# Optimization experiments

Measured on AMD Instinct MI355X. Metric: run time of the kernel, lower is better.

The kernel has to match this reference:

```python
import jax, jax.numpy as jnp
import numpy as np

B, L = 2, 2048          # batch, seq len (self-attention: M == L)
H, D, NB = 8, 16, 8     # n_heads, clifford_dim, n_blades (2^3 for sig_g=[1,1,1])
DM = H * D * NB         # d_model = 1024

# reverse() signs per blade for a 3D algebra, blade grades [0,1,1,1,2,2,2,3]:
# (-1)^{k(k-1)/2}; Euclidean metric signs from get_blade_signs are all +1,
# so the combined twist q_w = reverse(q) * signs is just these per-blade signs.
REV_SIGNS = jnp.array([1., 1., 1., 1., -1., -1., -1., -1.], dtype=jnp.float32)


def setup_inputs() -> dict:
    key = jax.random.key(0)
    ks = jax.random.split(key, 7)
    s = 1.0 / np.sqrt(DM)
    return {
        "query": jax.random.normal(ks[0], (B, L, DM), dtype=jnp.float32),
        "Wq": jax.random.normal(ks[1], (DM, DM), dtype=jnp.float32) * s,
        "bq": jax.random.normal(ks[2], (DM,), dtype=jnp.float32) * s,
        "Wk": jax.random.normal(ks[3], (DM, DM), dtype=jnp.float32) * s,
        "bk": jax.random.normal(ks[4], (DM,), dtype=jnp.float32) * s,
        "Wv": jax.random.normal(ks[5], (DM, DM), dtype=jnp.float32) * s,
        "bv": jax.random.normal(ks[6], (DM,), dtype=jnp.float32) * s,
    }


def reference(query, Wq, bq, Wk, bk, Wv, bv):
    b, l, _ = query.shape
    # projections (torch Linear: x @ W^T + b), reshape to (B,H,L,D,NB)
    def proj(x, W, bias):
        y = x @ W.T + bias
        return y.reshape(b, l, H, D, NB).transpose(0, 2, 1, 3, 4)

    q = proj(query, Wq, bq)
    k = proj(query, Wk, bk)   # self-attention: key = value = query
    v = proj(query, Wv, bv)

    q_w = q * REV_SIGNS  # reverse + blade-sign twist (elementwise over blade axis)
    scale = 1.0 / np.sqrt(D * NB)
    logits = jnp.einsum('bhldi,bhmdi->bhlm', q_w, k) * scale
    attn = jax.nn.softmax(logits, axis=-1)
    out = jnp.einsum('bhlm,bhmdi->bhldi', attn, v)
    out = out.transpose(0, 2, 1, 3, 4).reshape(b, l, -1)
    return out, attn.mean(axis=1)  # need_weights=True path
```

## Files before the change

kernel.cpp:

```cpp
#include <hip/hip_runtime.h>

typedef __attribute__((ext_vector_type(8))) __bf16 bf16x8;
typedef __attribute__((ext_vector_type(4))) __bf16 bf16x4;
typedef __attribute__((ext_vector_type(4))) float f32x4;
typedef __attribute__((ext_vector_type(16))) float f32x16;
typedef __attribute__((ext_vector_type(8))) unsigned short us8;
typedef __attribute__((ext_vector_type(4))) unsigned int u32x4;

constexpr float SCALE_L2E = 0.08838834764831845f * 1.4426950408889634f;

__device__ __forceinline__ unsigned short f2bf(float f) {
  unsigned int u = __float_as_uint(f);
  u = (u + 0x7FFFu + ((u >> 16) & 1u)) >> 16;
  return (unsigned short)u;
}

__device__ __forceinline__ void gl_lds16(const void* g, void* l) {
  __builtin_amdgcn_global_load_lds(
      (__attribute__((address_space(1))) void*)const_cast<void*>(g),
      (__attribute__((address_space(3))) void*)l, 16, 0, 0);
}

__global__ __launch_bounds__(256) void k_convert(
    const float* __restrict__ q, const float* __restrict__ wq,
    const float* __restrict__ wk, const float* __restrict__ wv,
    unsigned short* __restrict__ xb, unsigned short* __restrict__ wb) {
  long i = ((long)blockIdx.x * 256 + threadIdx.x) * 8;
  const float* s; unsigned short* d;
  if (i < 4194304)      { s = q  + i;             d = xb + i; }
  else if (i < 5242880) { s = wq + (i - 4194304); d = wb + (i - 4194304); }
  else if (i < 6291456) { s = wk + (i - 5242880); d = wb + 1048576 + (i - 5242880); }
  else                  { s = wv + (i - 6291456); d = wb + 2097152 + (i - 6291456); }
  float4 a = *(const float4*)s;
  float4 b = *(const float4*)(s + 4);
  us8 r;
  r[0]=f2bf(a.x); r[1]=f2bf(a.y); r[2]=f2bf(a.z); r[3]=f2bf(a.w);
  r[4]=f2bf(b.x); r[5]=f2bf(b.y); r[6]=f2bf(b.z); r[7]=f2bf(b.w);
  *(us8*)d = r;
}

__global__ __launch_bounds__(256) void k_proj(
    const unsigned short* __restrict__ xb, const unsigned short* __restrict__ wb,
    const float* __restrict__ bq, const float* __restrict__ bk, const float* __restrict__ bv,
    unsigned short* __restrict__ oq, unsigned short* __restrict__ ok_, unsigned short* __restrict__ vt) {
  __shared__ unsigned short As[4096];
  __shared__ unsigned short Bs[4096];
  const int t = threadIdx.x;
  const int wave = t >> 6, lane = t & 63;
  const int lrow = lane & 15, grp = lane >> 4;
  const int z = blockIdx.z;
  const unsigned short* w = wb + (size_t)z * 1048576;
  const float* bias = (z == 0) ? bq : ((z == 1) ? bk : bv);

  const unsigned short* asrc = xb + ((size_t)(blockIdx.y * 128 + (t >> 2)) * 1024 + (t & 3) * 8);
  const unsigned short* bsrc = w  + ((size_t)(blockIdx.x * 128 + (t >> 2)) * 1024 + (t & 3) * 8);

  f32x4 acc[4][4] = {};
  for (int kt = 0; kt < 32; ++kt) {
    gl_lds16(asrc + kt*32,              &As[t*8]);
    gl_lds16(asrc + kt*32 + 64*1024,    &As[2048 + t*8]);
    gl_lds16(bsrc + kt*32,              &Bs[t*8]);
    gl_lds16(bsrc + kt*32 + 64*1024,    &Bs[2048 + t*8]);
    __syncthreads();
    const int wr = wave >> 1, wc = wave & 1;
    bf16x8 af[4], bf[4];
#pragma unroll
    for (int mf = 0; mf < 4; ++mf)
      af[mf] = *(const bf16x8*)&As[(wr*64 + mf*16 + lrow)*32 + grp*8];
#pragma unroll
    for (int nf = 0; nf < 4; ++nf)
      bf[nf] = *(const bf16x8*)&Bs[(wc*64 + nf*16 + lrow)*32 + grp*8];
#pragma unroll
    for (int mf = 0; mf < 4; ++mf)
#pragma unroll
      for (int nf = 0; nf < 4; ++nf)
        acc[mf][nf] = __builtin_amdgcn_mfma_f32_16x16x32_bf16(af[mf], bf[nf], acc[mf][nf], 0, 0, 0);
    __syncthreads();
  }
  const int wr = wave >> 1, wc = wave & 1;
  if (z == 2) {
#pragma unroll
    for (int nf = 0; nf < 4; ++nf) {
      const int col = blockIdx.x*128 + wc*64 + nf*16 + lrow;
      const int h = col >> 7, dd = col & 127;
      const int dt = dd >> 5, lv = dd & 31;
      const float bsv = bias[col];
#pragma unroll
      for (int mf = 0; mf < 4; ++mf) {
        const int r0 = blockIdx.y*128 + wr*64 + mf*16 + grp*4;
        const int bb = r0 >> 11, m = r0 & 2047;
        const int mc = m >> 4, him = (m >> 3) & 1, j0 = m & 7;
        bf16x4 pv;
#pragma unroll
        for (int i = 0; i < 4; ++i) pv[i] = (__bf16)(acc[mf][nf][i] + bsv);
        const size_t off = ((((size_t)((bb*8 + h)*4 + dt))*128 + mc)*64 + lv + 32*him)*8 + j0;
        *(bf16x4*)&vt[off] = pv;
      }
    }
  } else {
    unsigned short* dst = (z == 0) ? oq : ok_;
    const float sign = (z == 0 && (lane & 7) >= 4) ? -1.0f : 1.0f;
#pragma unroll
    for (int nf = 0; nf < 4; ++nf) {
      const int col = blockIdx.x*128 + wc*64 + nf*16 + lrow;
      const float bsv = bias[col];
#pragma unroll
      for (int mf = 0; mf < 4; ++mf)
#pragma unroll
        for (int i = 0; i < 4; ++i) {
          const int row = blockIdx.y*128 + wr*64 + mf*16 + grp*4 + i;
          dst[(size_t)row*1024 + col] = f2bf((acc[mf][nf][i] + bsv) * sign);
        }
    }
  }
}

__global__ __launch_bounds__(256) void k_repack(const unsigned short* __restrict__ kws,
                                                unsigned short* __restrict__ kfrag) {
  const int c = blockIdx.x * 256 + threadIdx.x;
  const int lane = c & 63, kc = (c >> 6) & 7, mtile = (c >> 9) & 63, bh = c >> 15;
  const int b = bh >> 3, h = bh & 7;
  const int m = mtile*32 + (lane & 31);
  const int kd = kc*16 + (lane >> 5)*8;
  us8 v = *(const us8*)&kws[((size_t)(b*2048 + m))*1024 + h*128 + kd];
  *(us8*)&kfrag[(size_t)c * 8] = v;
}

__global__ __launch_bounds__(256) void k_attn_out(
    const unsigned short* __restrict__ qw, const unsigned short* __restrict__ kfrag,
    const unsigned short* __restrict__ vfrag, float* __restrict__ outp,
    float* __restrict__ rsw) {
  __shared__ __align__(16) char pool[65536];
  unsigned short (*KsL)[8192] = (unsigned short(*)[8192])pool;
  unsigned short (*VsL)[8192] = (unsigned short(*)[8192])(pool + 32768);
  float (*slab)[32][36] = (float(*)[32][36])pool;
  float (*rsred)[32] = (float(*)[32])(pool + 61440);
  float* invb = (float*)(pool + 62464);

  const int bid = blockIdx.x;
  const int xcd = bid & 7, r_ = bid >> 3;
  const int bh = (xcd << 1) | (r_ & 1);
  const int lt = r_ >> 1;
  const int b = bh >> 3, h = bh & 7;
  const int t = threadIdx.x;
  const int wave = t >> 6, lane = t & 63;
  const int mg = wave >> 1, lg = wave & 1;
  const int lm = lane & 31, hi = lane >> 5;

  bf16x8 qf[8];
  {
    const unsigned short* qp = qw + ((size_t)(b*2048 + lt*64 + lg*32 + lm))*1024
                                  + (size_t)h*128 + hi*8;
#pragma unroll
    for (int kc = 0; kc < 8; ++kc) qf[kc] = *(const bf16x8*)(qp + kc*16);
  }

  const unsigned short* kbp = kfrag + (size_t)bh*262144;
  const unsigned short* vbp = vfrag + (size_t)bh*262144;
  const int vdt = (t >> 6) & 3, vln = (t & 63) * 8;

  auto STAGE = [&](int buf, int it) {
#pragma unroll
    for (int q = 0; q < 2; ++q)
#pragma unroll
      for (int p = 0; p < 2; ++p)
        gl_lds16(kbp + (q*32 + it)*4096 + (p*256 + t)*8, &KsL[buf][q*4096 + (p*256 + t)*8]);
#pragma unroll
    for (int s = 0; s < 2; ++s)
#pragma unroll
      for (int w2 = 0; w2 < 2; ++w2)
        gl_lds16(vbp + vdt*65536 + (s*64 + it*2 + w2)*512 + vln,
                 &VsL[buf][s*4096 + w2*2048 + vdt*512 + vln]);
  };

  f32x16 oacc[4] = {};
  float rs = 0.f;

  STAGE(0, 0);
  __syncthreads();

  for (int it = 0; it < 32; ++it) {
    const int cur = it & 1;
    if (it + 1 < 32) STAGE(cur ^ 1, it + 1);

    bf16x8 kf[8];
#pragma unroll
    for (int kc = 0; kc < 8; ++kc)
      kf[kc] = *(const bf16x8*)&KsL[cur][mg*4096 + kc*512 + lane*8];
    f32x16 s = {};
#pragma unroll
    for (int kc = 0; kc < 8; ++kc)
      s = __builtin_amdgcn_mfma_f32_32x32x16_bf16(kf[kc], qf[kc], s, 0, 0, 0);

    bf16x8 vf[8];
#pragma unroll
    for (int w2 = 0; w2 < 2; ++w2)
#pragma unroll
      for (int dt = 0; dt < 4; ++dt)
        vf[w2*4 + dt] = *(const bf16x8*)&VsL[cur][mg*4096 + w2*2048 + dt*512 + lane*8];

    float e[16];
#pragma unroll
    for (int r = 0; r < 16; ++r) e[r] = __builtin_amdgcn_exp2f(s[r] * SCALE_L2E);
    float ps = 0.f;
#pragma unroll
    for (int r = 0; r < 16; ++r) ps += e[r];
    rs += ps;

    bf16x8 pf[2];
#pragma unroll
    for (int w2 = 0; w2 < 2; ++w2) {
      unsigned a0, a1, b0, b1;
      asm("v_cvt_pk_bf16_f32 %0, %1, %2" : "=v"(a0) : "v"(e[8*w2+0]), "v"(e[8*w2+1]));
      asm("v_cvt_pk_bf16_f32 %0, %1, %2" : "=v"(a1) : "v"(e[8*w2+2]), "v"(e[8*w2+3]));
      asm("v_cvt_pk_bf16_f32 %0, %1, %2" : "=v"(b0) : "v"(e[8*w2+4]), "v"(e[8*w2+5]));
      asm("v_cvt_pk_bf16_f32 %0, %1, %2" : "=v"(b1) : "v"(e[8*w2+6]), "v"(e[8*w2+7]));
      asm("v_permlane32_swap_b32 %0, %1" : "+v"(a0), "+v"(b0));
      asm("v_permlane32_swap_b32 %0, %1" : "+v"(a1), "+v"(b1));
      u32x4 pw = {a0, a1, b0, b1};
      pf[w2] = __builtin_bit_cast(bf16x8, pw);
    }

#pragma unroll
    for (int dt = 0; dt < 4; ++dt) {
      oacc[dt] = __builtin_amdgcn_mfma_f32_32x32x16_bf16(vf[dt],     pf[0], oacc[dt], 0, 0, 0);
      oacc[dt] = __builtin_amdgcn_mfma_f32_32x32x16_bf16(vf[4 + dt], pf[1], oacc[dt], 0, 0, 0);
    }
    __syncthreads();
  }

  rs += __shfl_xor(rs, 32, 64);
  if (lane < 32) rsred[wave][lm] = rs;
  __syncthreads();
  if (t < 64) {
    const int tlg = t >> 5, tl = t & 31;
    const float tot = rsred[tlg][tl] + rsred[2 + tlg][tl];
    rsw[(size_t)bh*2048 + lt*64 + t] = tot;
    invb[t] = 1.0f / tot;
  }

#pragma unroll
  for (int dt = 0; dt < 4; ++dt) {
    __syncthreads();
#pragma unroll
    for (int c = 0; c < 4; ++c) {
      float4 v4 = { oacc[dt][4*c + 0], oacc[dt][4*c + 1], oacc[dt][4*c + 2], oacc[dt][4*c + 3] };
      *(float4*)&slab[wave][lm][8*c + 4*hi] = v4;
    }
    __syncthreads();
    const int lgg = t >> 7, idx = t & 127;
    const int l = idx >> 2, d0 = (idx & 3) * 8;
    const float iv = invb[lgg*32 + l];
    float4 x0 = *(const float4*)&slab[lgg][l][d0];
    float4 x1 = *(const float4*)&slab[lgg][l][d0 + 4];
    float4 y0 = *(const float4*)&slab[2 + lgg][l][d0];
    float4 y1 = *(const float4*)&slab[2 + lgg][l][d0 + 4];
    float4 o0 = { (x0.x + y0.x)*iv, (x0.y + y0.y)*iv, (x0.z + y0.z)*iv, (x0.w + y0.w)*iv };
    float4 o1 = { (x1.x + y1.x)*iv, (x1.y + y1.y)*iv, (x1.z + y1.z)*iv, (x1.w + y1.w)*iv };
    float* op = outp + ((size_t)(b*2048 + lt*64 + lgg*32 + l))*1024 + h*128 + dt*32 + d0;
    *(float4*)op = o0;
    *(float4*)(op + 4) = o1;
  }
}

__global__ __launch_bounds__(512) void k_attn_mean(
    const unsigned short* __restrict__ qw, const unsigned short* __restrict__ kfrag,
    const float* __restrict__ rsw, float* __restrict__ meanp) {
  __shared__ unsigned short KsL[32768];
  __shared__ float slab[8][32][36];
  __shared__ float inv_s[256];
  const int bid = blockIdx.x;
  const int xcd = bid & 7, lt = bid >> 3;
  const int b = xcd >> 2, ms = xcd & 3;
  const int t = threadIdx.x;
  const int h = t >> 6, lane = t & 63;
  const int lm = lane & 31, hi = lane >> 5;

  if (t < 256) inv_s[t] = 1.0f / rsw[(size_t)(b*8 + (t>>5))*2048 + lt*32 + (t&31)];

  bf16x8 qf[8];
  {
    const unsigned short* qp = qw + ((size_t)(b*2048 + lt*32 + lm))*1024 + h*128 + hi*8;
#pragma unroll
    for (int kc = 0; kc < 8; ++kc) qf[kc] = *(const bf16x8*)(qp + kc*16);
  }

  auto STAGE = [&](int it) {
#pragma unroll
    for (int i = 0; i < 8; ++i) {
      const int c = i*512 + t;
      const int hh = c >> 9;
      gl_lds16(kfrag + (size_t)(b*8 + hh)*262144 + (size_t)(ms*16 + it)*4096 + (c & 511)*8,
               &KsL[c*8]);
    }
  };

  auto REDUCE = [&](int it) {
    const int m = t & 31, lp = t >> 5;
#pragma unroll
    for (int j = 0; j < 2; ++j) {
      const int l = lp*2 + j;
      float sum = 0.f;
#pragma unroll
      for (int w = 0; w < 8; ++w) sum += slab[w][m][l];
      meanp[(size_t)(b*2048 + lt*32 + l)*2048 + (ms*16 + it)*32 + m] = sum * 0.125f;
    }
  };

  STAGE(0);
  __syncthreads();

  float iv_r[16];
#pragma unroll
  for (int r = 0; r < 16; ++r)
    iv_r[r] = inv_s[h*32 + ((r & 3) + 8*(r >> 2) + 4*hi)];

  for (int it = 0; it < 16; ++it) {
    bf16x8 kf[8];
#pragma unroll
    for (int kc = 0; kc < 8; ++kc)
      kf[kc] = *(const bf16x8*)&KsL[(h*8 + kc)*512 + lane*8];
    f32x16 s = {};
#pragma unroll
    for (int kc = 0; kc < 8; ++kc)
      s = __builtin_amdgcn_mfma_f32_32x32x16_bf16(qf[kc], kf[kc], s, 0, 0, 0);

    float e[16];
#pragma unroll
    for (int r = 0; r < 16; ++r)
      e[r] = __builtin_amdgcn_exp2f(s[r] * SCALE_L2E) * iv_r[r];

#pragma unroll
    for (int gq = 0; gq < 4; ++gq) {
      float4 v4 = { e[gq*4 + 0], e[gq*4 + 1], e[gq*4 + 2], e[gq*4 + 3] };
      *(float4*)&slab[h][lm][gq*8 + hi*4] = v4;
    }
    __syncthreads();

    if (it + 1 < 16) STAGE(it + 1);
    REDUCE(it);
    __syncthreads();
  }
}

extern "C" void kernel_launch(void* const* d_in, const int* in_sizes, int n_in,
                              void* d_out, int out_size, void* d_ws, size_t ws_size,
                              hipStream_t stream) {
  (void)in_sizes; (void)n_in; (void)out_size; (void)ws_size;
  const float* query = (const float*)d_in[0];
  const float* Wq = (const float*)d_in[1];
  const float* bq = (const float*)d_in[2];
  const float* Wk = (const float*)d_in[3];
  const float* bk = (const float*)d_in[4];
  const float* Wv = (const float*)d_in[5];
  const float* bv = (const float*)d_in[6];
  float* outp  = (float*)d_out;
  float* meanp = outp + 4194304;

  char* ws = (char*)d_ws;
  unsigned short* xb    = (unsigned short*)(ws);
  unsigned short* wb    = (unsigned short*)(ws + 8388608);
  unsigned short* qws   = (unsigned short*)(ws + 14680064);
  unsigned short* kws   = (unsigned short*)(ws + 23068672);
  unsigned short* kfrag = (unsigned short*)(ws + 31457280);
  unsigned short* vfrag = (unsigned short*)(ws + 39845888);
  float*          rsw   = (float*)(ws + 48234496);

  k_convert<<<3584, 256, 0, stream>>>(query, Wq, Wk, Wv, xb, wb);
  k_proj<<<dim3(8, 32, 3), 256, 0, stream>>>(xb, wb, bq, bk, bv, qws, kws, vfrag);
  k_repack<<<2048, 256, 0, stream>>>(kws, kfrag);
  k_attn_out<<<512, 256, 0, stream>>>(qws, kfrag, vfrag, outp, rsw);
  k_attn_mean<<<512, 512, 0, stream>>>(qws, kfrag, rsw, meanp);
}
```

Baseline: 149.3 us.

## Double-buffer K staging and pack attention-mean slab as bf16

The K tile staging for the attention-mean kernel now uses two LDS buffers and prefetches the next tile at the top of each iteration, so the global-to-LDS copy overlaps the MFMA and exp work. The per-head probability slab is also stored as packed bf16 pairs rather than fp32, which halves LDS traffic for the cross-head reduction. The cost is double the K LDS footprint, which may lower occupancy, and reduced precision in the averaged attention weights before they are summed. The inline REDUCE lambda is replaced by an unpacking reduction that writes two rows per thread.

```diff
diff --git a/kernel.cpp b/kernel.cpp
--- a/kernel.cpp
+++ b/kernel.cpp
@@ -266,8 +266,8 @@
 __global__ __launch_bounds__(512) void k_attn_mean(
     const unsigned short* __restrict__ qw, const unsigned short* __restrict__ kfrag,
     const float* __restrict__ rsw, float* __restrict__ meanp) {
-  __shared__ unsigned short KsL[32768];
-  __shared__ float slab[8][32][36];
+  __shared__ unsigned short KsL[2][32768];
+  __shared__ unsigned int slabu[8][32][18];
   __shared__ float inv_s[256];
   const int bid = blockIdx.x;
   const int xcd = bid & 7, lt = bid >> 3;
@@ -285,29 +285,17 @@
     for (int kc = 0; kc < 8; ++kc) qf[kc] = *(const bf16x8*)(qp + kc*16);
   }
 
-  auto STAGE = [&](int it) {
+  auto STAGE = [&](int buf, int it) {
 #pragma unroll
     for (int i = 0; i < 8; ++i) {
       const int c = i*512 + t;
       const int hh = c >> 9;
       gl_lds16(kfrag + (size_t)(b*8 + hh)*262144 + (size_t)(ms*16 + it)*4096 + (c & 511)*8,
-               &KsL[c*8]);
+               &KsL[buf][c*8]);
     }
   };
 
-  auto REDUCE = [&](int it) {
-    const int m = t & 31, lp = t >> 5;
-#pragma unroll
-    for (int j = 0; j < 2; ++j) {
-      const int l = lp*2 + j;
-      float sum = 0.f;
-#pragma unroll
-      for (int w = 0; w < 8; ++w) sum += slab[w][m][l];
-      meanp[(size_t)(b*2048 + lt*32 + l)*2048 + (ms*16 + it)*32 + m] = sum * 0.125f;
-    }
-  };
-
-  STAGE(0);
+  STAGE(0, 0);
   __syncthreads();
 
   float iv_r[16];
@@ -316,10 +304,13 @@
     iv_r[r] = inv_s[h*32 + ((r & 3) + 8*(r >> 2) + 4*hi)];
 
   for (int it = 0; it < 16; ++it) {
+    const int cur = it & 1;
+    if (it + 1 < 16) STAGE(cur ^ 1, it + 1);
+
     bf16x8 kf[8];
 #pragma unroll
     for (int kc = 0; kc < 8; ++kc)
-      kf[kc] = *(const bf16x8*)&KsL[(h*8 + kc)*512 + lane*8];
+      kf[kc] = *(const bf16x8*)&KsL[cur][(h*8 + kc)*512 + lane*8];
     f32x16 s = {};
 #pragma unroll
     for (int kc = 0; kc < 8; ++kc)
@@ -332,13 +323,27 @@
 
 #pragma unroll
     for (int gq = 0; gq < 4; ++gq) {
-      float4 v4 = { e[gq*4 + 0], e[gq*4 + 1], e[gq*4 + 2], e[gq*4 + 3] };
-      *(float4*)&slab[h][lm][gq*8 + hi*4] = v4;
-    }
-    __syncthreads();
-
-    if (it + 1 < 16) STAGE(it + 1);
-    REDUCE(it);
+      unsigned p0, p1;
+      asm("v_cvt_pk_bf16_f32 %0, %1, %2" : "=v"(p0) : "v"(e[gq*4+0]), "v"(e[gq*4+1]));
+      asm("v_cvt_pk_bf16_f32 %0, %1, %2" : "=v"(p1) : "v"(e[gq*4+2]), "v"(e[gq*4+3]));
+      uint2 w2; w2.x = p0; w2.y = p1;
+      *(uint2*)&slabu[h][lm][gq*4 + hi*2] = w2;
+    }
+    __syncthreads();
+
+    {
+      const int m = t & 31, lp = t >> 5;
+      float s0 = 0.f, s1 = 0.f;
+#pragma unroll
+      for (int w = 0; w < 8; ++w) {
+        const unsigned pv = slabu[w][m][lp];
+        s0 += __uint_as_float(pv << 16);
+        s1 += __uint_as_float(pv & 0xFFFF0000u);
+      }
+      float* op = meanp + (size_t)(b*2048 + lt*32 + 2*lp)*2048 + (ms*16 + it)*32 + m;
+      op[0]    = s0 * 0.125f;
+      op[2048] = s1 * 0.125f;
+    }
     __syncthreads();
   }
 }
```

Result: no change. 148.8 us (-0.4%).
